# Optimization experiments

Hardware: AMD Instinct MI355X
Metric: run time of the kernel (lower is better)

The kernel has to match this reference:

```python
import jax, jax.numpy as jnp
import numpy as np

EPS = 1e-6

def _feature(x):
    # phi(x) = concat(relu(x), relu(-x)) along the last dim: (b,h,n,d) -> (b,h,n,2d)
    return jnp.concatenate([jax.nn.relu(x), jax.nn.relu(-x)], axis=-1)

def setup_inputs() -> dict:
    key = jax.random.key(0)
    kq, kk, kv = jax.random.split(key, 3)
    shape = (4, 16, 8192, 64)  # (batch, heads, seq_len, dim)
    Q = jax.random.normal(kq, shape, dtype=jnp.float32)
    K = jax.random.normal(kk, shape, dtype=jnp.float32)
    V = jax.random.normal(kv, shape, dtype=jnp.float32)
    return {"Q": Q, "K": K, "V": V}

def reference(Q, K, V):
    Qf = _feature(Q)  # (b,h,n,2d)
    Kf = _feature(K)  # (b,h,n,2d)
    # KV outer-product reduction over sequence: (b,h,2d,m)
    KV = jnp.einsum('bhnd,bhnm->bhdm', Kf, V)
    out = jnp.einsum('bhnd,bhdm->bhnm', Qf, KV)  # (b,h,n,m)
    K_sum = Kf.sum(axis=2)  # (b,h,2d)
    normalizer = jnp.einsum('bhnd,bhd->bhn', Qf, K_sum)  # (b,h,n)
    return out / (normalizer[..., None] + EPS)
```

## Files before the change

### kernel.cpp

```cpp
#include <hip/hip_runtime.h>

typedef __bf16 bf16x8 __attribute__((ext_vector_type(8)));
typedef __bf16 bf16x4 __attribute__((ext_vector_type(4)));
typedef float f32x4 __attribute__((ext_vector_type(4)));

#define BH_TOT 64
#define SEQ 8192
#define DIM 64
#define NCH 16
#define CHN (SEQ / NCH)
#define ROWS 64
#define NR (CHN / ROWS)
#define KV_STRIDE 68
#define KV_ROWS 128

__global__ __launch_bounds__(512, 8) void fla_ph1(const float* __restrict__ K,
                                                  const float* __restrict__ V,
                                                  float* __restrict__ kvf) {
  const int blk = blockIdx.x;
  const int bh = blk / NCH;
  const int ch = blk % NCH;
  const float* Kp = K + (size_t)bh * SEQ * DIM + (size_t)ch * CHN * DIM;
  const float* Vp = V + (size_t)bh * SEQ * DIM + (size_t)ch * CHN * DIM;

  __shared__ __bf16 Kb[ROWS][68];
  __shared__ __bf16 Vb[ROWS][68];

  const int tid = threadIdx.x;
  const int lane = tid & 63;
  const int w = tid >> 6;
  const int quad = lane >> 4;
  const int col = lane & 15;

  const int r0 = tid >> 4;
  const int c0 = (tid & 15) << 2;
  const int off0 = r0 * DIM + c0;
  const int off1 = off0 + 32 * DIM;

  f32x4 acc[5];
#pragma unroll
  for (int nt = 0; nt < 5; ++nt) acc[nt] = (f32x4){0.f, 0.f, 0.f, 0.f};

  bf16x8 bones;
#pragma unroll
  for (int j = 0; j < 8; ++j) bones[j] = (__bf16)0.f;
  if (col == 0) {
#pragma unroll
    for (int j = 0; j < 8; ++j) bones[j] = (__bf16)1.0f;
  }

  const int kcol = ((w & 3) << 4) + col;
  const bool neg = (w >= 4);

  float4 pk0 = *(const float4*)(Kp + off0);
  float4 pk1 = *(const float4*)(Kp + off1);
  float4 pv0 = *(const float4*)(Vp + off0);
  float4 pv1 = *(const float4*)(Vp + off1);

  for (int s = 0; s < NR; ++s) {
    bf16x4 kb0, kb1, vb0, vb1;
    kb0[0] = (__bf16)pk0.x; kb0[1] = (__bf16)pk0.y; kb0[2] = (__bf16)pk0.z; kb0[3] = (__bf16)pk0.w;
    kb1[0] = (__bf16)pk1.x; kb1[1] = (__bf16)pk1.y; kb1[2] = (__bf16)pk1.z; kb1[3] = (__bf16)pk1.w;
    vb0[0] = (__bf16)pv0.x; vb0[1] = (__bf16)pv0.y; vb0[2] = (__bf16)pv0.z; vb0[3] = (__bf16)pv0.w;
    vb1[0] = (__bf16)pv1.x; vb1[1] = (__bf16)pv1.y; vb1[2] = (__bf16)pv1.z; vb1[3] = (__bf16)pv1.w;

    if (s + 1 < NR) {
      const float* Kn = Kp + (s + 1) * ROWS * DIM;
      const float* Vn = Vp + (s + 1) * ROWS * DIM;
      pk0 = *(const float4*)(Kn + off0);
      pk1 = *(const float4*)(Kn + off1);
      pv0 = *(const float4*)(Vn + off0);
      pv1 = *(const float4*)(Vn + off1);
    }

    __syncthreads();
    *(bf16x4*)&Kb[r0][c0]      = kb0;
    *(bf16x4*)&Kb[r0 + 32][c0] = kb1;
    *(bf16x4*)&Vb[r0][c0]      = vb0;
    *(bf16x4*)&Vb[r0 + 32][c0] = vb1;
    __syncthreads();

#pragma unroll
    for (int sl = 0; sl < 2; ++sl) {
      bf16x8 a;
#pragma unroll
      for (int j = 0; j < 8; ++j) {
        int rr = sl * 32 + quad * 8 + j;
        float kv = (float)Kb[rr][kcol];
        if (neg) kv = -kv;
        a[j] = (__bf16)fmaxf(kv, 0.f);
      }
#pragma unroll
      for (int nt = 0; nt < 4; ++nt) {
        bf16x8 b;
#pragma unroll
        for (int j = 0; j < 8; ++j)
          b[j] = Vb[sl * 32 + quad * 8 + j][col + nt * 16];
        acc[nt] = __builtin_amdgcn_mfma_f32_16x16x32_bf16(a, b, acc[nt], 0, 0, 0);
      }
      acc[4] = __builtin_amdgcn_mfma_f32_16x16x32_bf16(a, bones, acc[4], 0, 0, 0);
    }
  }

  float* dst = kvf + (size_t)bh * KV_ROWS * KV_STRIDE;
  const int feat = w * 16 + quad * 4;
#pragma unroll
  for (int nt = 0; nt < 5; ++nt) {
    int c = nt * 16 + col;
    if (c <= 64) {
#pragma unroll
      for (int r = 0; r < 4; ++r)
        atomicAdd(&dst[(size_t)(feat + r) * KV_STRIDE + c], acc[nt][r]);
    }
  }
}

__global__ __launch_bounds__(256) void fla_ph2(const float* __restrict__ Q,
                                               const float* __restrict__ kvf,
                                               float* __restrict__ out) {
  const int blk = blockIdx.x;
  const int bh = blk >> 5;
  const int rb = blk & 31;
  const float* Qp = Q + (size_t)bh * SEQ * DIM + (size_t)rb * 256 * DIM;
  float* Op = out + (size_t)bh * SEQ * DIM + (size_t)rb * 256 * DIM;

  __shared__ __bf16 kvb[128][66];
  const float* src = kvf + (size_t)bh * KV_ROWS * KV_STRIDE;
  for (int i = threadIdx.x; i < 128 * 66; i += 256) {
    int k = i / 66;
    int c = i - k * 66;
    float v = (c <= 64) ? src[(size_t)k * KV_STRIDE + c] : 0.f;
    kvb[k][c] = (__bf16)v;
  }
  __syncthreads();

  const int lane = threadIdx.x & 63;
  const int w = threadIdx.x >> 6;
  const int quad = lane >> 4;
  const int col = lane & 15;

  bf16x8 bfr[4][5];
#pragma unroll
  for (int kt = 0; kt < 4; ++kt) {
#pragma unroll
    for (int j = 0; j < 8; ++j) {
      int k = kt * 32 + quad * 8 + j;
      bfr[kt][0][j] = kvb[k][col];
      bfr[kt][1][j] = kvb[k][col + 16];
      bfr[kt][2][j] = kvb[k][col + 32];
      bfr[kt][3][j] = kvb[k][col + 48];
      bfr[kt][4][j] = (col == 0) ? kvb[k][64] : (__bf16)0.f;
    }
  }

#pragma unroll
  for (int mt = 0; mt < 4; ++mt) {
    const float* qrow = Qp + (size_t)(w * 64 + mt * 16 + col) * DIM;
    float4 q0 = *(const float4*)(qrow + quad * 8);
    float4 q1 = *(const float4*)(qrow + quad * 8 + 4);
    float4 q2 = *(const float4*)(qrow + 32 + quad * 8);
    float4 q3 = *(const float4*)(qrow + 32 + quad * 8 + 4);
    float qv[16];
    *(float4*)&qv[0] = q0;  *(float4*)&qv[4] = q1;
    *(float4*)&qv[8] = q2;  *(float4*)&qv[12] = q3;
    bf16x8 a0, a1, a2, a3;
#pragma unroll
    for (int j = 0; j < 8; ++j) {
      a0[j] = (__bf16)fmaxf(qv[j], 0.f);
      a2[j] = (__bf16)fmaxf(-qv[j], 0.f);
      a1[j] = (__bf16)fmaxf(qv[8 + j], 0.f);
      a3[j] = (__bf16)fmaxf(-qv[8 + j], 0.f);
    }
    f32x4 acc[5];
#pragma unroll
    for (int nt = 0; nt < 5; ++nt) acc[nt] = (f32x4){0.f, 0.f, 0.f, 0.f};
#pragma unroll
    for (int nt = 0; nt < 5; ++nt) {
      acc[nt] = __builtin_amdgcn_mfma_f32_16x16x32_bf16(a0, bfr[0][nt], acc[nt], 0, 0, 0);
      acc[nt] = __builtin_amdgcn_mfma_f32_16x16x32_bf16(a1, bfr[1][nt], acc[nt], 0, 0, 0);
      acc[nt] = __builtin_amdgcn_mfma_f32_16x16x32_bf16(a2, bfr[2][nt], acc[nt], 0, 0, 0);
      acc[nt] = __builtin_amdgcn_mfma_f32_16x16x32_bf16(a3, bfr[3][nt], acc[nt], 0, 0, 0);
    }
    float inv[4];
#pragma unroll
    for (int r = 0; r < 4; ++r) {
      float nrm = __shfl((float)acc[4][r], lane & 48, 64);
      inv[r] = 1.0f / (nrm + 1e-6f);
    }
    float* orow = Op + (size_t)(w * 64 + mt * 16) * DIM;
#pragma unroll
    for (int nt = 0; nt < 4; ++nt)
#pragma unroll
      for (int r = 0; r < 4; ++r)
        orow[(size_t)(quad * 4 + r) * DIM + nt * 16 + col] = acc[nt][r] * inv[r];
  }
}

extern "C" void kernel_launch(void* const* d_in, const int* in_sizes, int n_in,
                              void* d_out, int out_size, void* d_ws, size_t ws_size,
                              hipStream_t stream) {
  const float* Q = (const float*)d_in[0];
  const float* K = (const float*)d_in[1];
  const float* V = (const float*)d_in[2];
  float* out = (float*)d_out;
  float* kvf = (float*)d_ws;

  hipMemsetAsync(kvf, 0, (size_t)BH_TOT * KV_ROWS * KV_STRIDE * sizeof(float), stream);
  fla_ph1<<<dim3(BH_TOT * NCH), dim3(512), 0, stream>>>(K, V, kvf);
  fla_ph2<<<dim3(BH_TOT * 32), dim3(256), 0, stream>>>(Q, kvf, out);
}
```

Baseline: 457.5 us.

## Replace atomic KV accumulation with per-chunk partials and a bf16 reduction kernel

```diff
diff --git a/kernel.cpp b/kernel.cpp
--- a/kernel.cpp
+++ b/kernel.cpp
@@ -11,12 +11,15 @@
 #define CHN (SEQ / NCH)
 #define ROWS 64
 #define NR (CHN / ROWS)
-#define KV_STRIDE 68
+#define PART_STRIDE 68
 #define KV_ROWS 128
+#define RED_COLS 66
+
+#define PART_ELEMS ((size_t)BH_TOT * NCH * KV_ROWS * PART_STRIDE)
 
 __global__ __launch_bounds__(512, 8) void fla_ph1(const float* __restrict__ K,
                                                   const float* __restrict__ V,
-                                                  float* __restrict__ kvf) {
+                                                  float* __restrict__ kvp) {
   const int blk = blockIdx.x;
   const int bh = blk / NCH;
   const int ch = blk % NCH;
@@ -102,7 +105,7 @@
     }
   }
 
-  float* dst = kvf + (size_t)bh * KV_ROWS * KV_STRIDE;
+  float* dst = kvp + ((size_t)bh * NCH + ch) * KV_ROWS * PART_STRIDE;
   const int feat = w * 16 + quad * 4;
 #pragma unroll
   for (int nt = 0; nt < 5; ++nt) {
@@ -110,13 +113,31 @@
     if (c <= 64) {
 #pragma unroll
       for (int r = 0; r < 4; ++r)
-        atomicAdd(&dst[(size_t)(feat + r) * KV_STRIDE + c], acc[nt][r]);
-    }
-  }
+        dst[(size_t)(feat + r) * PART_STRIDE + c] = acc[nt][r];
+    }
+  }
+}
+
+__global__ __launch_bounds__(256) void fla_red(const float* __restrict__ kvp,
+                                               __bf16* __restrict__ kvr) {
+  const int idx = blockIdx.x * 256 + threadIdx.x;
+  const int bh = idx / (KV_ROWS * RED_COLS);
+  const int rem = idx - bh * (KV_ROWS * RED_COLS);
+  const int r = rem / RED_COLS;
+  const int c = rem - r * RED_COLS;
+  float s = 0.f;
+  if (c <= 64) {
+    const float* src = kvp + (size_t)bh * NCH * KV_ROWS * PART_STRIDE
+                     + (size_t)r * PART_STRIDE + c;
+#pragma unroll
+    for (int ch = 0; ch < NCH; ++ch)
+      s += src[(size_t)ch * KV_ROWS * PART_STRIDE];
+  }
+  kvr[idx] = (__bf16)s;
 }
 
 __global__ __launch_bounds__(256) void fla_ph2(const float* __restrict__ Q,
-                                               const float* __restrict__ kvf,
+                                               const __bf16* __restrict__ kvr,
                                                float* __restrict__ out) {
   const int blk = blockIdx.x;
   const int bh = blk >> 5;
@@ -124,13 +145,12 @@
   const float* Qp = Q + (size_t)bh * SEQ * DIM + (size_t)rb * 256 * DIM;
   float* Op = out + (size_t)bh * SEQ * DIM + (size_t)rb * 256 * DIM;
 
-  __shared__ __bf16 kvb[128][66];
-  const float* src = kvf + (size_t)bh * KV_ROWS * KV_STRIDE;
-  for (int i = threadIdx.x; i < 128 * 66; i += 256) {
-    int k = i / 66;
-    int c = i - k * 66;
-    float v = (c <= 64) ? src[(size_t)k * KV_STRIDE + c] : 0.f;
-    kvb[k][c] = (__bf16)v;
+  __shared__ __align__(16) __bf16 kvb[KV_ROWS][RED_COLS];
+  {
+    const f32x4* s = (const f32x4*)(kvr + (size_t)bh * KV_ROWS * RED_COLS);
+    f32x4* d = (f32x4*)&kvb[0][0];
+    for (int i = threadIdx.x; i < KV_ROWS * RED_COLS * 2 / 16; i += 256)
+      d[i] = s[i];
   }
   __syncthreads();
 
@@ -203,9 +223,10 @@
   const float* K = (const float*)d_in[1];
   const float* V = (const float*)d_in[2];
   float* out = (float*)d_out;
-  float* kvf = (float*)d_ws;
-
-  hipMemsetAsync(kvf, 0, (size_t)BH_TOT * KV_ROWS * KV_STRIDE * sizeof(float), stream);
-  fla_ph1<<<dim3(BH_TOT * NCH), dim3(512), 0, stream>>>(K, V, kvf);
-  fla_ph2<<<dim3(BH_TOT * 32), dim3(256), 0, stream>>>(Q, kvf, out);
-}
+  float* kvp = (float*)d_ws;
+  __bf16* kvr = (__bf16*)((float*)d_ws + PART_ELEMS);
+
+  fla_ph1<<<dim3(BH_TOT * NCH), dim3(512), 0, stream>>>(K, V, kvp);
+  fla_red<<<dim3(BH_TOT * KV_ROWS * RED_COLS / 256), dim3(256), 0, stream>>>(kvp, kvr);
+  fla_ph2<<<dim3(BH_TOT * 32), dim3(256), 0, stream>>>(Q, kvr, out);
+}
```

Measured after the change: 420.3 us. -8.1%, faster.
